# Kernel optimization log

Hardware: AMD Instinct MI355X
Metric: run time of the kernel (lower is better)

The kernel has to match this reference:

```python
import jax, jax.numpy as jnp
import numpy as np

N_GRID, N_IO = 99872, 128   # height*width, n_inputs+n_outputs
N = N_GRID + N_IO           # 100000 nodes
E = 1600000                 # edges before self-loops
HID, WID = 128, 128         # hidden_dim, network_width (heads=1)


def _ln(h, g, b, eps=1e-5):
    mu = jnp.mean(h, axis=-1, keepdims=True)
    v = jnp.mean((h - mu) ** 2, axis=-1, keepdims=True)
    return (h - mu) * jax.lax.rsqrt(v + eps) * g + b


def setup_inputs() -> dict:
    ks = jax.random.split(jax.random.key(0), 32)
    r = lambda i, sh, s=0.05: jax.random.normal(ks[i], sh, jnp.float32) * s
    return {
        "x": jax.random.normal(ks[0], (N, HID + 2), jnp.float32),
        "edge_index": jax.random.randint(ks[1], (2, E), 0, N),
        "initial": r(2, (N_IO, HID)),
        "Wf1": r(3, (HID + 2, WID)), "bf1": r(4, (WID,)),
        "Wf2": r(5, (WID, HID + 2)), "bf2": r(6, (HID + 2,)),
        "Wu1": r(7, (HID + 2, WID)), "bu1": r(8, (WID,)),
        "Wu2": r(9, (WID, HID)), "bu2": r(10, (HID,)),
        "Wc1": r(11, (HID + 2, WID)), "bc1": r(12, (WID,)),
        "Wc2": r(13, (WID, WID)), "bc2": r(14, (WID,)),
        "Wc3": r(15, (WID, WID)), "bc3": r(16, (WID,)),
        "Wc4": r(17, (WID, WID)), "bc4": r(18, (WID,)),
        "Wco": r(19, (WID, HID)), "bco": r(20, (HID,)),
        "g3": jnp.ones((WID,), jnp.float32), "bn3": jnp.zeros((WID,), jnp.float32),
        "g6": jnp.ones((WID,), jnp.float32), "bn6": jnp.zeros((WID,), jnp.float32),
        "g7": jnp.ones((WID,), jnp.float32), "bn7": jnp.zeros((WID,), jnp.float32),
    }


def _step(x, initial, Wf1, bf1, Wf2, bf2, Wu1, bu1, Wu2, bu2,
          Wc1, bc1, Wc2, bc2, Wc3, bc3, Wc4, bc4, Wco, bco,
          g3, bn3, g6, bn6, g7, bn7, edge_index):
    # GCNConv: add self-loops, symmetric deg^-1/2 normalization, max-aggregation.
    loops = jnp.arange(N)
    row = jnp.concatenate([edge_index[0], loops])  # source
    col = jnp.concatenate([edge_index[1], loops])  # target
    deg = jax.ops.segment_sum(jnp.ones(row.shape[0], x.dtype), col, num_segments=N)
    dinv = jnp.where(deg > 0, jax.lax.rsqrt(deg), 0.0)
    norm = dinv[row] * dinv[col]  # [E+N]

    def gcn(h, W, b):
        m = (h @ W)[row] * norm[:, None]                      # gather + scale
        return jax.ops.segment_max(m, col, num_segments=N) + b  # scatter-max

    # forget gate, mixing toward the (padded) initial state
    f = jax.nn.sigmoid(jax.nn.sigmoid(x @ Wf1 + bf1) @ Wf2 + bf2)  # [N, HID+2]
    init_pad = jnp.concatenate([jnp.zeros((N_GRID, HID), x.dtype), initial], axis=0)
    init_pad = jnp.concatenate([init_pad, jnp.zeros((N, 2), x.dtype)], axis=1)
    x = x * f + (1.0 - f) * init_pad

    # update gate
    u = jax.nn.sigmoid(jax.nn.sigmoid(x @ Wu1 + bu1) @ Wu2 + bu2)  # [N, HID]

    h = jax.nn.relu(_ln(gcn(x, Wc1, bc1), g3, bn3))
    h = _ln(gcn(h, Wc2, bc2), g3, bn3)   # layer_norm3 reused, as in source
    h = _ln(gcn(h, Wc3, bc3), g6, bn6)
    h = _ln(gcn(h, Wc4, bc4), g7, bn7)
    h = gcn(h, Wco, bco)                 # [N, HID]
    return x[:, :-2] + h * u


def reference(x, edge_index, initial, Wf1, bf1, Wf2, bf2, Wu1, bu1, Wu2, bu2,
              Wc1, bc1, Wc2, bc2, Wc3, bc3, Wc4, bc4, Wco, bco,
              g3, bn3, g6, bn6, g7, bn7):
    return _step(x, initial, Wf1, bf1, Wf2, bf2, Wu1, bu1, Wu2, bu2,
                 Wc1, bc1, Wc2, bc2, Wc3, bc3, Wc4, bc4, Wco, bco,
                 g3, bn3, g6, bn6, g7, bn7, edge_index)
```

## Files before the change

kernel.cpp:

```cpp
#include <hip/hip_runtime.h>
#include <cstdint>

#define HID 128
#define HC  130
#define NIO 128
#define DENSW 64
#define SUBB 8
#define BCAP_S 160

typedef _Float16 f16;
typedef _Float16 f16x2 __attribute__((ext_vector_type(2)));
typedef _Float16 f16x4 __attribute__((ext_vector_type(4)));
typedef _Float16 f16x8 __attribute__((ext_vector_type(8)));
typedef float    f32x4 __attribute__((ext_vector_type(4)));

__device__ __forceinline__ float sigm(float z) {
  return 1.0f / (1.0f + __expf(-z));
}

__device__ __forceinline__ int xcc_id() {
  int x;
  asm volatile("s_getreg_b32 %0, hwreg(HW_REG_XCC_ID)" : "=s"(x));
  return x & 7;
}

__device__ __forceinline__ f16x8 max8(f16x8 a, f16x8 b) {
  union P { f16x8 h; f16x2 p[4]; } A, B, O;
  A.h = a; B.h = b;
  #pragma unroll
  for (int i = 0; i < 4; ++i)
    asm("v_pk_max_f16 %0, %1, %2" : "=v"(O.p[i]) : "v"(A.p[i]), "v"(B.p[i]));
  return O.h;
}

__global__ void zero_int_kernel(int* __restrict__ p, int n) {
  int i = blockIdx.x * blockDim.x + threadIdx.x;
  if (i < n) p[i] = 0;
}

__global__ void binscatter_kernel(const int* __restrict__ row, const int* __restrict__ col,
    int* __restrict__ bcnt, unsigned* __restrict__ bucket, int e, int nb) {
  const int g0 = xcc_id() * SUBB + ((blockIdx.x >> 3) & (SUBB - 1));
  int i = blockIdx.x * blockDim.x + threadIdx.x;
  if (i >= e) return;
  int c = col[i], r = row[i];
  int b = c >> 7;
  int cur = atomicAdd(&bcnt[g0 * nb + b], 1);
  if (cur < BCAP_S)
    bucket[((size_t)g0 * nb + b) * BCAP_S + cur] = ((unsigned)r << 7) | (unsigned)(c & 127);
}

__global__ __launch_bounds__(256) void build_kernel(const int* __restrict__ bcnt,
    const unsigned* __restrict__ bucket, int* __restrict__ ncnt,
    int* __restrict__ dense, float* __restrict__ dinv, int n, int nb) {
  __shared__ int lcnt[128];
  const int b = blockIdx.x;
  const int t = threadIdx.x;
  if (t < 128) lcnt[t] = 0;
  __syncthreads();
  const int wv = t >> 6, ln = t & 63;
  #pragma unroll 1
  for (int g = wv * 16; g < wv * 16 + 16; ++g) {
    const int cntg = min(bcnt[g * nb + b], BCAP_S);
    const unsigned* __restrict__ src = bucket + ((size_t)g * nb + b) * BCAP_S;
    for (int idx = ln; idx < cntg; idx += 64) {
      unsigned ev = src[idx];
      int cl = (int)(ev & 127u);
      int r  = (int)(ev >> 7);
      int s = atomicAdd(&lcnt[cl], 1);
      if (s < DENSW) dense[(size_t)((b << 7) + cl) * DENSW + s] = r;
    }
  }
  __syncthreads();
  if (t < 128) {
    int c = (b << 7) + t;
    if (c < n) {
      int cc = min(lcnt[t], DENSW);
      ncnt[c] = cc;
      dinv[c] = rsqrtf((float)(cc + 1));
    }
  }
}

struct WDesc { const float* src; f16* dst; int K, NC, Kpad, NCpad; };
struct WAll { WDesc m[9]; };

__global__ __launch_bounds__(256) void wprep_kernel(WAll wa) {
  const WDesc d = wa.m[blockIdx.y];
  const int KST = d.Kpad >> 5;
  const int total = (d.NCpad >> 4) * KST * 64;
  int idx = blockIdx.x * 256 + threadIdx.x;
  if (idx >= total) return;
  int nt  = idx / (KST * 64);
  int rem = idx - nt * (KST * 64);
  int ks  = rem >> 6;
  int l   = rem & 63;
  int n   = nt * 16 + (l & 15);
  int k0  = ks * 32 + (l >> 4) * 8;
  f16x8 o;
  #pragma unroll
  for (int j = 0; j < 8; ++j) {
    int k = k0 + j;
    float v = (k < d.K && n < d.NC) ? d.src[(size_t)k * d.NC + n] : 0.0f;
    o[j] = (f16)v;
  }
  *((f16x8*)d.dst + idx) = o;
}

__global__ void xprep_kernel(const float* __restrict__ x, f16* __restrict__ x16,
                             f16* __restrict__ xg, int n) {
  int idx = blockIdx.x * blockDim.x + threadIdx.x;
  if (idx >= n * 160) return;
  int r = idx / 160, c = idx - r * 160;
  x16[idx] = (f16)((c < 130) ? x[(size_t)r * 130 + c] : 0.0f);
  if (c >= 130) xg[idx] = (f16)0.0f;
}

template<int KPAD, int RS, int NCPAD, int NC, int MODE>
__global__ __launch_bounds__(256, 4) void mm_mfma(
    const f16* __restrict__ X, const f16* __restrict__ Wt,
    const float* __restrict__ bias, f16* __restrict__ Y,
    const float* __restrict__ dinv, const f16* __restrict__ xor16,
    const float* __restrict__ initial, int n, int ngrid)
{
  constexpr int KST = KPAD / 32;
  constexpr int NT  = NCPAD / 16;
  constexpr int YRS = (MODE == 1) ? 160 : 128;
  constexpr int PSTR = (NCPAD == 128) ? 132 : 148;
  constexpr int LDSH = (NCPAD * KPAD > 128 * PSTR) ? NCPAD * KPAD : 128 * PSTR;
  __shared__ __align__(16) f16 Bs[LDSH];

  const int t = threadIdx.x;
  const int wid  = t >> 6;
  const int l    = t & 63;
  const int m15  = l & 15;
  const int quad = l >> 4;
  const int rw   = blockIdx.x * 128 + wid * 32;

  constexpr int BSW = NCPAD * KPAD / 8;
  #pragma unroll
  for (int i = 0; i < (BSW + 255) / 256; ++i) {
    int idx = t + i * 256;
    if (BSW % 256 == 0 || idx < BSW)
      ((f16x8*)Bs)[idx] = ((const f16x8*)Wt)[idx];
  }

  const f16* Xr0 = X + (size_t)(rw + m15) * RS;
  const f16* Xr1 = X + (size_t)(rw + 16 + m15) * RS;
  f16x8 a0r[KST], a1r[KST];
  #pragma unroll
  for (int ks = 0; ks < KST; ++ks) {
    const int off = ks * 32 + quad * 8;
    a0r[ks] = *(const f16x8*)(Xr0 + off);
    a1r[ks] = *(const f16x8*)(Xr1 + off);
  }

  const int r  = t >> 1;
  const int hf = t & 1;
  const int gr = blockIdx.x * 128 + r;
  float dv = 0.0f;
  if constexpr (MODE == 2) dv = (gr < n) ? dinv[gr] : 0.0f;

  f16x8 xo[8];
  f16x2 xo2;
  if constexpr (MODE == 1) {
    const f16* xp = xor16 + (size_t)(blockIdx.x * 128 + r) * 160;
    #pragma unroll
    for (int c8 = 0; c8 < 8; ++c8)
      xo[c8] = *(const f16x8*)(xp + hf * 64 + c8 * 8);
    xo2 = *(const f16x2*)(xp + 128);
  }

  __syncthreads();

  f32x4 acc[2][NT];
  #pragma unroll
  for (int mt = 0; mt < 2; ++mt)
    #pragma unroll
    for (int nt = 0; nt < NT; ++nt)
      acc[mt][nt] = (f32x4){0.f, 0.f, 0.f, 0.f};

  #pragma unroll
  for (int ks = 0; ks < KST; ++ks) {
    #pragma unroll
    for (int nt = 0; nt < NT; ++nt) {
      f16x8 b = *((const f16x8*)Bs + (nt * KST + ks) * 64 + l);
      acc[0][nt] = __builtin_amdgcn_mfma_f32_16x16x32_f16(a0r[ks], b, acc[0][nt], 0, 0, 0);
      acc[1][nt] = __builtin_amdgcn_mfma_f32_16x16x32_f16(a1r[ks], b, acc[1][nt], 0, 0, 0);
    }
  }

  __syncthreads();

  #pragma unroll
  for (int mt = 0; mt < 2; ++mt) {
    #pragma unroll
    for (int reg = 0; reg < 4; ++reg) {
      const int rl = wid * 32 + mt * 16 + quad * 4 + reg;
      #pragma unroll
      for (int nt = 0; nt < NT; ++nt)
        Bs[rl * PSTR + nt * 16 + m15] = (f16)acc[mt][nt][reg];
    }
  }
  __syncthreads();

  if (gr < n) {
    if constexpr (MODE == 0 || MODE == 2) {
      #pragma unroll
      for (int c8 = 0; c8 < 8; ++c8) {
        const int c0 = hf * 64 + c8 * 8;
        f16x8 v = *(const f16x8*)&Bs[r * PSTR + c0];
        f16x8 o;
        #pragma unroll
        for (int j = 0; j < 8; ++j) {
          float a = (float)v[j];
          if constexpr (MODE == 0) o[j] = (f16)sigm(a + bias[c0 + j]);
          else                     o[j] = (f16)(a * dv);
        }
        *(f16x8*)&Y[(size_t)gr * YRS + c0] = o;
      }
    } else {
      const bool hasInit = (gr >= ngrid);
      #pragma unroll
      for (int c8 = 0; c8 < 8; ++c8) {
        const int c0 = hf * 64 + c8 * 8;
        f16x8 v = *(const f16x8*)&Bs[r * PSTR + c0];
        f16x8 o;
        #pragma unroll
        for (int j = 0; j < 8; ++j) {
          const int col = c0 + j;
          float fv = sigm((float)v[j] + bias[col]);
          float xov = (float)xo[c8][j];
          float ip = hasInit ? initial[(size_t)(gr - ngrid) * 128 + col] : 0.0f;
          o[j] = (f16)(xov * fv + (1.0f - fv) * ip);
        }
        *(f16x8*)&Y[(size_t)gr * YRS + c0] = o;
      }
      if (hf) {
        #pragma unroll
        for (int k = 0; k < 2; ++k) {
          const int col = 128 + k;
          float fv = sigm((float)Bs[r * PSTR + col] + bias[col]);
          Y[(size_t)gr * YRS + col] = (f16)((float)xo2[k] * fv);
        }
      }
    }
  }
}

template<int K1PAD, int RS1, int NC2PAD, int NC2, int MODE2>
__global__ __launch_bounds__(256, 2) void mm_fused(
    const f16* __restrict__ X, const f16* __restrict__ W1t, const f16* __restrict__ W2t,
    const float* __restrict__ b1, const float* __restrict__ b2, f16* __restrict__ Y,
    const f16* __restrict__ xor16, const float* __restrict__ initial, int n, int ngrid)
{
  constexpr int KST1 = K1PAD / 32;
  constexpr int NT1  = 8;
  constexpr int KST2 = 4;
  constexpr int NT2  = NC2PAD / 16;
  constexpr int PSTR1 = 132;
  constexpr int PSTR2 = (NC2PAD == 128) ? 132 : 148;
  constexpr int YRS  = (MODE2 == 1) ? 160 : 128;
  constexpr int W2U  = NC2PAD * 128;
  constexpr int SC_A = K1PAD * 128;
  constexpr int SC_B = 128 * PSTR2;
  constexpr int SCU  = (SC_A > SC_B) ? SC_A : SC_B;
  __shared__ __align__(16) f16 L[W2U + SCU];
  f16* Bs2 = L;
  f16* SC  = L + W2U;

  const int t = threadIdx.x;
  const int wid  = t >> 6;
  const int l    = t & 63;
  const int m15  = l & 15;
  const int quad = l >> 4;
  const int rw   = blockIdx.x * 128 + wid * 32;

  constexpr int W1W = K1PAD * 128 / 8;
  constexpr int W2W = NC2PAD * 128 / 8;
  for (int i = t; i < W1W; i += 256) ((f16x8*)SC)[i]  = ((const f16x8*)W1t)[i];
  for (int i = t; i < W2W; i += 256) ((f16x8*)Bs2)[i] = ((const f16x8*)W2t)[i];

  const f16* Xr0 = X + (size_t)(rw + m15) * RS1;
  const f16* Xr1 = X + (size_t)(rw + 16 + m15) * RS1;
  f16x8 a0r[KST1], a1r[KST1];
  #pragma unroll
  for (int ks = 0; ks < KST1; ++ks) {
    const int off = ks * 32 + quad * 8;
    a0r[ks] = *(const f16x8*)(Xr0 + off);
    a1r[ks] = *(const f16x8*)(Xr1 + off);
  }

  f16x8 xo[8];
  f16x2 xo2;
  if constexpr (MODE2 == 1) {
    const f16* xp = xor16 + (size_t)(blockIdx.x * 128 + (t >> 1)) * 160;
    #pragma unroll
    for (int c8 = 0; c8 < 8; ++c8)
      xo[c8] = *(const f16x8*)(xp + (t & 1) * 64 + c8 * 8);
    xo2 = *(const f16x2*)(xp + 128);
  }

  float b1r[NT1];
  #pragma unroll
  for (int nt = 0; nt < NT1; ++nt) b1r[nt] = b1[nt * 16 + m15];

  __syncthreads();

  f32x4 acc1[2][NT1];
  #pragma unroll
  for (int mt = 0; mt < 2; ++mt)
    #pragma unroll
    for (int nt = 0; nt < NT1; ++nt)
      acc1[mt][nt] = (f32x4){0.f, 0.f, 0.f, 0.f};

  #pragma unroll
  for (int ks = 0; ks < KST1; ++ks) {
    #pragma unroll
    for (int nt = 0; nt < NT1; ++nt) {
      f16x8 b = *((const f16x8*)SC + (nt * KST1 + ks) * 64 + l);
      acc1[0][nt] = __builtin_amdgcn_mfma_f32_16x16x32_f16(a0r[ks], b, acc1[0][nt], 0, 0, 0);
      acc1[1][nt] = __builtin_amdgcn_mfma_f32_16x16x32_f16(a1r[ks], b, acc1[1][nt], 0, 0, 0);
    }
  }

  __syncthreads();

  #pragma unroll
  for (int mt = 0; mt < 2; ++mt) {
    #pragma unroll
    for (int reg = 0; reg < 4; ++reg) {
      const int rl = wid * 32 + mt * 16 + quad * 4 + reg;
      #pragma unroll
      for (int nt = 0; nt < NT1; ++nt)
        SC[rl * PSTR1 + nt * 16 + m15] = (f16)sigm(acc1[mt][nt][reg] + b1r[nt]);
    }
  }
  __syncthreads();

  f32x4 acc2[2][NT2];
  #pragma unroll
  for (int mt = 0; mt < 2; ++mt)
    #pragma unroll
    for (int nt = 0; nt < NT2; ++nt)
      acc2[mt][nt] = (f32x4){0.f, 0.f, 0.f, 0.f};

  const int rA0 = wid * 32 + m15;
  const int rA1 = rA0 + 16;
  union A8 { f16x8 v; f16x4 q[2]; };
  #pragma unroll
  for (int ks = 0; ks < KST2; ++ks) {
    const int k0 = ks * 32 + quad * 8;
    A8 a0, a1;
    a0.q[0] = *(const f16x4*)&SC[rA0 * PSTR1 + k0];
    a0.q[1] = *(const f16x4*)&SC[rA0 * PSTR1 + k0 + 4];
    a1.q[0] = *(const f16x4*)&SC[rA1 * PSTR1 + k0];
    a1.q[1] = *(const f16x4*)&SC[rA1 * PSTR1 + k0 + 4];
    #pragma unroll
    for (int nt = 0; nt < NT2; ++nt) {
      f16x8 b = *((const f16x8*)Bs2 + (nt * KST2 + ks) * 64 + l);
      acc2[0][nt] = __builtin_amdgcn_mfma_f32_16x16x32_f16(a0.v, b, acc2[0][nt], 0, 0, 0);
      acc2[1][nt] = __builtin_amdgcn_mfma_f32_16x16x32_f16(a1.v, b, acc2[1][nt], 0, 0, 0);
    }
  }
  __syncthreads();

  #pragma unroll
  for (int mt = 0; mt < 2; ++mt) {
    #pragma unroll
    for (int reg = 0; reg < 4; ++reg) {
      const int rl = wid * 32 + mt * 16 + quad * 4 + reg;
      #pragma unroll
      for (int nt = 0; nt < NT2; ++nt)
        SC[rl * PSTR2 + nt * 16 + m15] = (f16)acc2[mt][nt][reg];
    }
  }
  __syncthreads();

  const int r  = t >> 1;
  const int hf = t & 1;
  const int gr = blockIdx.x * 128 + r;
  if (gr < n) {
    if constexpr (MODE2 == 0) {
      #pragma unroll
      for (int c8 = 0; c8 < 8; ++c8) {
        const int c0 = hf * 64 + c8 * 8;
        f16x8 v = *(const f16x8*)&SC[r * PSTR2 + c0];
        f16x8 o;
        #pragma unroll
        for (int j = 0; j < 8; ++j)
          o[j] = (f16)sigm((float)v[j] + b2[c0 + j]);
        *(f16x8*)&Y[(size_t)gr * YRS + c0] = o;
      }
    } else {
      const bool hasInit = (gr >= ngrid);
      #pragma unroll
      for (int c8 = 0; c8 < 8; ++c8) {
        const int c0 = hf * 64 + c8 * 8;
        f16x8 v = *(const f16x8*)&SC[r * PSTR2 + c0];
        f16x8 o;
        #pragma unroll
        for (int j = 0; j < 8; ++j) {
          const int col = c0 + j;
          float fv = sigm((float)v[j] + b2[col]);
          float xov = (float)xo[c8][j];
          float ip = hasInit ? initial[(size_t)(gr - ngrid) * 128 + col] : 0.0f;
          o[j] = (f16)(xov * fv + (1.0f - fv) * ip);
        }
        *(f16x8*)&Y[(size_t)gr * YRS + c0] = o;
      }
      if (hf) {
        #pragma unroll
        for (int k = 0; k < 2; ++k) {
          const int col = 128 + k;
          float fv = sigm((float)SC[r * PSTR2 + col] + b2[col]);
          Y[(size_t)gr * YRS + col] = (f16)((float)xo2[k] * fv);
        }
      }
    }
  }
}

template<int MODE>
__global__ __launch_bounds__(256) void agg_kernel(
    const f16* __restrict__ G, const int* __restrict__ ncnt,
    const int* __restrict__ dense,
    const float* __restrict__ dinv, const float* __restrict__ bias,
    const float* __restrict__ gamma, const float* __restrict__ beta,
    const f16* __restrict__ xg, const f16* __restrict__ u,
    void* __restrict__ out, int n)
{
  const int wid = threadIdx.x >> 6, lane = threadIdx.x & 63;
  const int c = blockIdx.x * 4 + wid;
  if (c >= n) return;
  const int li = lane & 15, grp = lane >> 4;

  union F8 { f16x8 h; int4 i; };
  const int nc = min(ncnt[c], DENSW);
  const int raw = dense[(size_t)c * DENSW + lane];
  const int myidx = (lane < nc) ? raw : c;

  F8 m; m.h = *(const f16x8*)(G + (size_t)c * 128 + li * 8);
  F8 m2; m2.h = m.h;
  F8 m3; m3.h = m.h;
  F8 m4; m4.h = m.h;
  const int B = (nc + 3) >> 2;
  int b = 0;
  for (; b + 3 < B; b += 4) {
    int r0 = __shfl(myidx, (b + 0) * 4 + grp, 64);
    int r1 = __shfl(myidx, (b + 1) * 4 + grp, 64);
    int r2 = __shfl(myidx, (b + 2) * 4 + grp, 64);
    int r3 = __shfl(myidx, (b + 3) * 4 + grp, 64);
    F8 v0; v0.h = *(const f16x8*)(G + (size_t)r0 * 128 + li * 8);
    F8 v1; v1.h = *(const f16x8*)(G + (size_t)r1 * 128 + li * 8);
    F8 v2; v2.h = *(const f16x8*)(G + (size_t)r2 * 128 + li * 8);
    F8 v3; v3.h = *(const f16x8*)(G + (size_t)r3 * 128 + li * 8);
    m.h  = max8(m.h,  v0.h);
    m2.h = max8(m2.h, v1.h);
    m3.h = max8(m3.h, v2.h);
    m4.h = max8(m4.h, v3.h);
  }
  for (; b < B; ++b) {
    int r0 = __shfl(myidx, b * 4 + grp, 64);
    F8 v; v.h = *(const f16x8*)(G + (size_t)r0 * 128 + li * 8);
    m.h = max8(m.h, v.h);
  }
  m.h = max8(max8(m.h, m2.h), max8(m3.h, m4.h));

  #pragma unroll
  for (int st = 16; st <= 32; st <<= 1) {
    F8 o;
    #pragma unroll
    for (int d = 0; d < 4; ++d) o.i[d] = __shfl_xor(m.i[d], st, 64);
    m.h = max8(m.h, o.h);
  }

  const float dc = dinv[c];
  float v[8];
  float s = 0.f, sq = 0.f;
  #pragma unroll
  for (int j = 0; j < 8; ++j) {
    v[j] = (float)m.h[j] * dc + bias[li * 8 + j];
    s += v[j]; sq += v[j] * v[j];
  }

  if constexpr (MODE == 2) {
    if (grp == 0) {
      f16x8 xv = *(const f16x8*)(xg + (size_t)c * 160 + li * 8);
      f16x8 uv = *(const f16x8*)(u  + (size_t)c * 128 + li * 8);
      float o[8];
      #pragma unroll
      for (int j = 0; j < 8; ++j) o[j] = (float)xv[j] + v[j] * (float)uv[j];
      float* op = (float*)out + (size_t)c * 128 + li * 8;
      *(float4*)op       = make_float4(o[0], o[1], o[2], o[3]);
      *(float4*)(op + 4) = make_float4(o[4], o[5], o[6], o[7]);
    }
  } else {
    #pragma unroll
    for (int st = 1; st <= 8; st <<= 1) {
      s  += __shfl_xor(s, st, 64);
      sq += __shfl_xor(sq, st, 64);
    }
    float mu  = s * (1.0f / 128.0f);
    float var = sq * (1.0f / 128.0f) - mu * mu;
    float rstd = rsqrtf(var + 1e-5f);
    if (grp == 0) {
      f16x8 ov;
      #pragma unroll
      for (int j = 0; j < 8; ++j) {
        float o = (v[j] - mu) * rstd * gamma[li * 8 + j] + beta[li * 8 + j];
        if constexpr (MODE == 0) o = fmaxf(o, 0.0f);
        ov[j] = (f16)o;
      }
      *(f16x8*)((f16*)out + (size_t)c * 128 + li * 8) = ov;
    }
  }
}

extern "C" void kernel_launch(void* const* d_in, const int* in_sizes, int n_in,
                              void* d_out, int out_size, void* d_ws, size_t ws_size,
                              hipStream_t stream) {
  (void)n_in; (void)out_size; (void)ws_size;
  const float* x       = (const float*)d_in[0];
  const int*   ei      = (const int*)d_in[1];
  const float* initial = (const float*)d_in[2];
  const float* Wf1 = (const float*)d_in[3];  const float* bf1 = (const float*)d_in[4];
  const float* Wf2 = (const float*)d_in[5];  const float* bf2 = (const float*)d_in[6];
  const float* Wu1 = (const float*)d_in[7];  const float* bu1 = (const float*)d_in[8];
  const float* Wu2 = (const float*)d_in[9];  const float* bu2 = (const float*)d_in[10];
  const float* Wc1 = (const float*)d_in[11]; const float* bc1 = (const float*)d_in[12];
  const float* Wc2 = (const float*)d_in[13]; const float* bc2 = (const float*)d_in[14];
  const float* Wc3 = (const float*)d_in[15]; const float* bc3 = (const float*)d_in[16];
  const float* Wc4 = (const float*)d_in[17]; const float* bc4 = (const float*)d_in[18];
  const float* Wco = (const float*)d_in[19]; const float* bco = (const float*)d_in[20];
  const float* g3  = (const float*)d_in[21]; const float* bn3 = (const float*)d_in[22];
  const float* g6  = (const float*)d_in[23]; const float* bn6 = (const float*)d_in[24];
  const float* g7  = (const float*)d_in[25]; const float* bn7 = (const float*)d_in[26];

  const int N  = in_sizes[0] / HC;
  const int E  = in_sizes[1] / 2;
  const int NG = N - NIO;
  const int NP = N + 128;
  const int NB = (N + 127) / 128;
  const int NSEG = 8 * SUBB;

  char* w = (char*)d_ws;
  auto carve = [&](size_t bytes) {
    char* p = w; w += (bytes + 255) & ~(size_t)255; return p;
  };
  int*      bcnt   = (int*)     carve((size_t)NB * NSEG * 4);
  unsigned* bucket = (unsigned*)carve((size_t)NB * NSEG * BCAP_S * 4);
  int*      ncnt   = (int*)     carve((size_t)N * 4);
  int*      dense  = (int*)     carve((size_t)N * DENSW * 4);
  float*    dinv   = (float*)   carve((size_t)N * 4);
  f16*      x16    = (f16*)     carve((size_t)NP * 160 * 2);
  f16*      S      = (f16*)     carve((size_t)NP * 128 * 2);
  f16*      xg     = (f16*)     carve((size_t)NP * 160 * 2);
  f16*      u      = (f16*)     carve((size_t)N  * 128 * 2);
  f16*      G      = (f16*)     carve((size_t)N  * 128 * 2);
  f16*      H      = (f16*)     carve((size_t)NP * 128 * 2);
  f16*      Wt_f1  = (f16*)     carve(160 * 128 * 2);
  f16*      Wt_f2  = (f16*)     carve(128 * 144 * 2);
  f16*      Wt_u1  = (f16*)     carve(160 * 128 * 2);
  f16*      Wt_u2  = (f16*)     carve(128 * 128 * 2);
  f16*      Wt_c1  = (f16*)     carve(160 * 128 * 2);
  f16*      Wt_c2  = (f16*)     carve(128 * 128 * 2);
  f16*      Wt_c3  = (f16*)     carve(128 * 128 * 2);
  f16*      Wt_c4  = (f16*)     carve(128 * 128 * 2);
  f16*      Wt_co  = (f16*)     carve(128 * 128 * 2);
  (void)S;

  const int* erow = ei;
  const int* ecol = ei + E;

  const int gE = (E + 255) / 256;
  const int gM = (N + 127) / 128;
  const int gA = (N + 3) / 4;

  WAll wa;
  wa.m[0] = {Wf1, Wt_f1, HC,  HID, 160, 128};
  wa.m[1] = {Wf2, Wt_f2, HID, HC,  128, 144};
  wa.m[2] = {Wu1, Wt_u1, HC,  HID, 160, 128};
  wa.m[3] = {Wu2, Wt_u2, HID, HID, 128, 128};
  wa.m[4] = {Wc1, Wt_c1, HC,  HID, 160, 128};
  wa.m[5] = {Wc2, Wt_c2, HID, HID, 128, 128};
  wa.m[6] = {Wc3, Wt_c3, HID, HID, 128, 128};
  wa.m[7] = {Wc4, Wt_c4, HID, HID, 128, 128};
  wa.m[8] = {Wco, Wt_co, HID, HID, 128, 128};
  wprep_kernel<<<dim3(10, 9), 256, 0, stream>>>(wa);
  xprep_kernel<<<(N * 160 + 255) / 256, 256, 0, stream>>>(x, x16, xg, N);

  zero_int_kernel<<<(NB * NSEG + 255) / 256, 256, 0, stream>>>(bcnt, NB * NSEG);
  binscatter_kernel<<<gE, 256, 0, stream>>>(erow, ecol, bcnt, bucket, E, NB);
  build_kernel<<<NB, 256, 0, stream>>>(bcnt, bucket, ncnt, dense, dinv, N, NB);

  mm_fused<160, 160, 144, 130, 1><<<gM, 256, 0, stream>>>(
      x16, Wt_f1, Wt_f2, bf1, bf2, xg, x16, initial, N, NG);
  mm_fused<160, 160, 128, 128, 0><<<gM, 256, 0, stream>>>(
      xg, Wt_u1, Wt_u2, bu1, bu2, u, nullptr, nullptr, N, NG);

  mm_mfma<160, 160, 128, 128, 2><<<gM, 256, 0, stream>>>(xg, Wt_c1, nullptr, G, dinv, nullptr, nullptr, N, NG);
  agg_kernel<0><<<gA, 256, 0, stream>>>(G, ncnt, dense, dinv, bc1, g3, bn3, nullptr, nullptr, H, N);
  mm_mfma<128, 128, 128, 128, 2><<<gM, 256, 0, stream>>>(H, Wt_c2, nullptr, G, dinv, nullptr, nullptr, N, NG);
  agg_kernel<1><<<gA, 256, 0, stream>>>(G, ncnt, dense, dinv, bc2, g3, bn3, nullptr, nullptr, H, N);
  mm_mfma<128, 128, 128, 128, 2><<<gM, 256, 0, stream>>>(H, Wt_c3, nullptr, G, dinv, nullptr, nullptr, N, NG);
  agg_kernel<1><<<gA, 256, 0, stream>>>(G, ncnt, dense, dinv, bc3, g6, bn6, nullptr, nullptr, H, N);
  mm_mfma<128, 128, 128, 128, 2><<<gM, 256, 0, stream>>>(H, Wt_c4, nullptr, G, dinv, nullptr, nullptr, N, NG);
  agg_kernel<1><<<gA, 256, 0, stream>>>(G, ncnt, dense, dinv, bc4, g7, bn7, nullptr, nullptr, H, N);
  mm_mfma<128, 128, 128, 128, 2><<<gM, 256, 0, stream>>>(H, Wt_co, nullptr, G, dinv, nullptr, nullptr, N, NG);
  agg_kernel<2><<<gA, 256, 0, stream>>>(G, ncnt, dense, dinv, bco, nullptr, nullptr, xg, u, d_out, N);
}
```

Measured before the change: 745.7 us.

## Merge prep kernels into one launch, vectorize x conversion, trim bucket capacity

Merges the weight-prep, x-prep and counter-zeroing kernels into a single launch that selects its role by block index. The x conversion now handles 8 columns per thread with vectorized f16x8 stores instead of one element per thread. The per-bucket capacity shrinks from 160 to 128, and the aggregation kernel loads the upper half of the neighbor list only when a node has more than 32 neighbors. The smaller bucket capacity risks dropping edges if any sub-bucket overflows 128 entries.

```diff
diff --git a/kernel.cpp b/kernel.cpp
--- a/kernel.cpp
+++ b/kernel.cpp
@@ -6,7 +6,7 @@
 #define NIO 128
 #define DENSW 64
 #define SUBB 8
-#define BCAP_S 160
+#define BCAP_S 128
 
 typedef _Float16 f16;
 typedef _Float16 f16x2 __attribute__((ext_vector_type(2)));
@@ -33,9 +33,58 @@
   return O.h;
 }
 
-__global__ void zero_int_kernel(int* __restrict__ p, int n) {
-  int i = blockIdx.x * blockDim.x + threadIdx.x;
-  if (i < n) p[i] = 0;
+struct WDesc { const float* src; f16* dst; int K, NC, Kpad, NCpad; };
+struct WAll { WDesc m[9]; };
+
+__global__ __launch_bounds__(256) void prep_kernel(
+    const float* __restrict__ x, f16* __restrict__ x16, f16* __restrict__ xg,
+    int n, WAll wa, int* __restrict__ bcnt, int nzero, int gX) {
+  const int bb = blockIdx.x;
+  const int t = threadIdx.x;
+  if (bb < gX) {
+    int idx = bb * 256 + t;
+    if (idx >= n * 20) return;
+    int r = idx / 20, g = idx - r * 20;
+    int c0 = g * 8;
+    f16x8 o;
+    #pragma unroll
+    for (int j = 0; j < 8; ++j) {
+      int c = c0 + j;
+      o[j] = (f16)((c < HC) ? x[(size_t)r * HC + c] : 0.0f);
+    }
+    *(f16x8*)&x16[(size_t)r * 160 + c0] = o;
+    if (c0 >= 136) {
+      f16x8 z = (f16x8){0,0,0,0,0,0,0,0};
+      *(f16x8*)&xg[(size_t)r * 160 + c0] = z;
+    } else if (c0 == 128) {
+      #pragma unroll
+      for (int c = 130; c < 136; ++c) xg[(size_t)r * 160 + c] = (f16)0.0f;
+    }
+  } else if (bb < gX + 90) {
+    const int wb = bb - gX;
+    const WDesc d = wa.m[wb / 10];
+    const int KST = d.Kpad >> 5;
+    const int total = (d.NCpad >> 4) * KST * 64;
+    int idx = (wb % 10) * 256 + t;
+    if (idx >= total) return;
+    int nt  = idx / (KST * 64);
+    int rem = idx - nt * (KST * 64);
+    int ks  = rem >> 6;
+    int l   = rem & 63;
+    int nn  = nt * 16 + (l & 15);
+    int k0  = ks * 32 + (l >> 4) * 8;
+    f16x8 o;
+    #pragma unroll
+    for (int j = 0; j < 8; ++j) {
+      int k = k0 + j;
+      float v = (k < d.K && nn < d.NC) ? d.src[(size_t)k * d.NC + nn] : 0.0f;
+      o[j] = (f16)v;
+    }
+    *((f16x8*)d.dst + idx) = o;
+  } else {
+    int i = (bb - gX - 90) * 256 + t;
+    if (i < nzero) bcnt[i] = 0;
+  }
 }
 
 __global__ void binscatter_kernel(const int* __restrict__ row, const int* __restrict__ col,
@@ -80,40 +129,6 @@
       dinv[c] = rsqrtf((float)(cc + 1));
     }
   }
-}
-
-struct WDesc { const float* src; f16* dst; int K, NC, Kpad, NCpad; };
-struct WAll { WDesc m[9]; };
-
-__global__ __launch_bounds__(256) void wprep_kernel(WAll wa) {
-  const WDesc d = wa.m[blockIdx.y];
-  const int KST = d.Kpad >> 5;
-  const int total = (d.NCpad >> 4) * KST * 64;
-  int idx = blockIdx.x * 256 + threadIdx.x;
-  if (idx >= total) return;
-  int nt  = idx / (KST * 64);
-  int rem = idx - nt * (KST * 64);
-  int ks  = rem >> 6;
-  int l   = rem & 63;
-  int n   = nt * 16 + (l & 15);
-  int k0  = ks * 32 + (l >> 4) * 8;
-  f16x8 o;
-  #pragma unroll
-  for (int j = 0; j < 8; ++j) {
-    int k = k0 + j;
-    float v = (k < d.K && n < d.NC) ? d.src[(size_t)k * d.NC + n] : 0.0f;
-    o[j] = (f16)v;
-  }
-  *((f16x8*)d.dst + idx) = o;
-}
-
-__global__ void xprep_kernel(const float* __restrict__ x, f16* __restrict__ x16,
-                             f16* __restrict__ xg, int n) {
-  int idx = blockIdx.x * blockDim.x + threadIdx.x;
-  if (idx >= n * 160) return;
-  int r = idx / 160, c = idx - r * 160;
-  x16[idx] = (f16)((c < 130) ? x[(size_t)r * 130 + c] : 0.0f);
-  if (c >= 130) xg[idx] = (f16)0.0f;
 }
 
 template<int KPAD, int RS, int NCPAD, int NC, int MODE>
@@ -437,7 +452,11 @@
 
   union F8 { f16x8 h; int4 i; };
   const int nc = min(ncnt[c], DENSW);
-  const int raw = dense[(size_t)c * DENSW + lane];
+  int raw = 0;
+  if (lane < 32) raw = dense[(size_t)c * DENSW + lane];
+  if (nc > 32) {
+    if (lane >= 32) raw = dense[(size_t)c * DENSW + lane];
+  }
   const int myidx = (lane < nc) ? raw : c;
 
   F8 m; m.h = *(const f16x8*)(G + (size_t)c * 128 + li * 8);
@@ -554,7 +573,6 @@
   int*      dense  = (int*)     carve((size_t)N * DENSW * 4);
   float*    dinv   = (float*)   carve((size_t)N * 4);
   f16*      x16    = (f16*)     carve((size_t)NP * 160 * 2);
-  f16*      S      = (f16*)     carve((size_t)NP * 128 * 2);
   f16*      xg     = (f16*)     carve((size_t)NP * 160 * 2);
   f16*      u      = (f16*)     carve((size_t)N  * 128 * 2);
   f16*      G      = (f16*)     carve((size_t)N  * 128 * 2);
@@ -568,7 +586,6 @@
   f16*      Wt_c3  = (f16*)     carve(128 * 128 * 2);
   f16*      Wt_c4  = (f16*)     carve(128 * 128 * 2);
   f16*      Wt_co  = (f16*)     carve(128 * 128 * 2);
-  (void)S;
 
   const int* erow = ei;
   const int* ecol = ei + E;
@@ -587,10 +604,10 @@
   wa.m[6] = {Wc3, Wt_c3, HID, HID, 128, 128};
   wa.m[7] = {Wc4, Wt_c4, HID, HID, 128, 128};
   wa.m[8] = {Wco, Wt_co, HID, HID, 128, 128};
-  wprep_kernel<<<dim3(10, 9), 256, 0, stream>>>(wa);
-  xprep_kernel<<<(N * 160 + 255) / 256, 256, 0, stream>>>(x, x16, xg, N);
-
-  zero_int_kernel<<<(NB * NSEG + 255) / 256, 256, 0, stream>>>(bcnt, NB * NSEG);
+  const int gX = (N * 20 + 255) / 256;
+  const int gZ = (NB * NSEG + 255) / 256;
+  prep_kernel<<<gX + 90 + gZ, 256, 0, stream>>>(x, x16, xg, N, wa, bcnt, NB * NSEG, gX);
+
   binscatter_kernel<<<gE, 256, 0, stream>>>(erow, ecol, bcnt, bucket, E, NB);
   build_kernel<<<NB, 256, 0, stream>>>(bcnt, bucket, ncnt, dense, dinv, N, NB);
 
```

New measurement: 738.7 us. Within noise of the previous version (-0.9%).
